# Performance work log

Measured on AMD Instinct MI355X. Metric: run time of the kernel, lower is better.

The kernel has to match this reference:

```python
import jax, jax.numpy as jnp
import numpy as np

B, L, Q, K, H = 64, 1024, 1024, 1024, 1024

def setup_inputs() -> dict:
    key = jax.random.key(0)
    k1, k2, k3, k4, k5, k6 = jax.random.split(key, 6)
    query = jax.random.normal(k1, (B, Q), dtype=jnp.float32)
    keys = jax.random.normal(k2, (B, L, K), dtype=jnp.float32)
    mask = jax.random.randint(k3, (B, L), 0, 2).astype(bool)
    # nn.Linear weights: W1 [H, Q], W2 [H, K], v [1, H], all bias-free
    W1 = jax.random.normal(k4, (H, Q), dtype=jnp.float32) / np.sqrt(Q)
    W2 = jax.random.normal(k5, (H, K), dtype=jnp.float32) / np.sqrt(K)
    v = jax.random.normal(k6, (1, H), dtype=jnp.float32) / np.sqrt(H)
    return {"query": query, "keys": keys, "mask": mask, "W1": W1, "W2": W2, "v": v}

def reference(query, keys, mask, W1, W2, v):
    # q: [B, H], broadcast over seq dim instead of expand
    q = query @ W1.T                                  # [B, H]
    k = jnp.einsum('blk,hk->blh', keys, W2)           # [B, L, H]
    scores = jnp.tanh(q[:, None, :] + k) @ v[0]       # [B, L]
    scores = jnp.where(mask, -jnp.inf, scores)
    weights = jax.nn.softmax(scores, axis=-1)
    weights = jnp.nan_to_num(weights, nan=0.0)
    context = jnp.einsum('bl,blk->bk', weights, keys) # [B, K]
    return (context, weights)
```

## Files before the change

### kernel.cpp

```cpp
#include <hip/hip_runtime.h>
#include <math.h>


typedef __attribute__((ext_vector_type(8))) short short8;
typedef __attribute__((ext_vector_type(4))) float floatx4;

__device__ __forceinline__ short f2bf(float x) {
    unsigned u = __float_as_uint(x);
    u += 0x7fffu + ((u >> 16) & 1u);
    return (short)(u >> 16);
}
__device__ __forceinline__ short8 pack8(float4 lo, float4 hi) {
    short8 r;
    r[0]=f2bf(lo.x); r[1]=f2bf(lo.y); r[2]=f2bf(lo.z); r[3]=f2bf(lo.w);
    r[4]=f2bf(hi.x); r[5]=f2bf(hi.y); r[6]=f2bf(hi.z); r[7]=f2bf(hi.w);
    return r;
}
__device__ __forceinline__ float fast_tanh(float x) {
    const float e = __expf(2.f * x);
    return 1.f - 2.f * __builtin_amdgcn_rcpf(e + 1.f);
}

#define LDA 40

__global__ __launch_bounds__(256) void k0_zero(float* __restrict__ out) {
    const int i = (blockIdx.x * 256 + threadIdx.x) * 4;
    const float4 z = {0.f, 0.f, 0.f, 0.f};
    *(float4*)(out + i) = z;
}

__global__ __launch_bounds__(256) void k1_qproj(
    const float* __restrict__ query, const float* __restrict__ W1,
    float* __restrict__ out)
{
    __shared__ float As[32][64];
    __shared__ float Bs[32][64];
    const int t  = threadIdx.x;
    const int tx = t & 15, ty = t >> 4;
    const int h0 = blockIdx.x * 64;
    const int kbase = blockIdx.y * 256;
    const int sr = t >> 2;
    const int sk = (t & 3) * 8;
    float c[4][4] = {{0.f}};
    for (int k0 = kbase; k0 < kbase + 256; k0 += 32) {
        const float4 a0 = *(const float4*)(query + sr * 1024 + k0 + sk);
        const float4 a1 = *(const float4*)(query + sr * 1024 + k0 + sk + 4);
        const float4 b0 = *(const float4*)(W1 + (h0 + sr) * 1024 + k0 + sk);
        const float4 b1 = *(const float4*)(W1 + (h0 + sr) * 1024 + k0 + sk + 4);
        __syncthreads();
        As[sk+0][sr]=a0.x; As[sk+1][sr]=a0.y; As[sk+2][sr]=a0.z; As[sk+3][sr]=a0.w;
        As[sk+4][sr]=a1.x; As[sk+5][sr]=a1.y; As[sk+6][sr]=a1.z; As[sk+7][sr]=a1.w;
        Bs[sk+0][sr]=b0.x; Bs[sk+1][sr]=b0.y; Bs[sk+2][sr]=b0.z; Bs[sk+3][sr]=b0.w;
        Bs[sk+4][sr]=b1.x; Bs[sk+5][sr]=b1.y; Bs[sk+6][sr]=b1.z; Bs[sk+7][sr]=b1.w;
        __syncthreads();
        #pragma unroll
        for (int k = 0; k < 32; ++k) {
            const float4 av = *(const float4*)&As[k][ty*4];
            const float4 bv = *(const float4*)&Bs[k][tx*4];
            const float aa[4] = {av.x, av.y, av.z, av.w};
            const float bb[4] = {bv.x, bv.y, bv.z, bv.w};
            #pragma unroll
            for (int i = 0; i < 4; ++i)
                #pragma unroll
                for (int j = 0; j < 4; ++j)
                    c[i][j] = fmaf(aa[i], bb[j], c[i][j]);
        }
    }
    #pragma unroll
    for (int i = 0; i < 4; ++i)
        #pragma unroll
        for (int j = 0; j < 4; ++j)
            atomicAdd(&out[(ty*4 + i) * 1024 + h0 + tx*4 + j], c[i][j]);
}

__global__ __launch_bounds__(256) void k_pack(const float* __restrict__ src,
                                              short* __restrict__ dst, int npanels)
{
    __shared__ short sm[16][1032];
    const int t = threadIdx.x;
    for (int p = blockIdx.x; p < npanels; p += gridDim.x) {
        const float* s = src + (size_t)p * 16 * 1024;
        short* d = dst + (size_t)p * 16 * 1024;
        __syncthreads();
        #pragma unroll
        for (int it = 0; it < 8; ++it) {
            const int idx = it * 256 + t;
            const int row = idx >> 7;
            const int c8  = idx & 127;
            const float4 a = *(const float4*)(s + row * 1024 + c8 * 8);
            const float4 b = *(const float4*)(s + row * 1024 + c8 * 8 + 4);
            *(short8*)&sm[row][c8 * 8] = pack8(a, b);
        }
        __syncthreads();
        #pragma unroll
        for (int it = 0; it < 8; ++it) {
            const int u = it * 256 + t;
            const int m = u & 15, c = u >> 4;
            ((short8*)d)[u] = *(const short8*)&sm[m][c * 8];
        }
    }
}

__global__ __launch_bounds__(256) void k2_scores_full(
    const short* __restrict__ keysp, const short* __restrict__ W2p,
    const float* __restrict__ v, float* __restrict__ out)
{
    __shared__ float red[128][33];
    const int t  = threadIdx.x;
    const int l0 = blockIdx.x * 128;
    const int b  = blockIdx.y;
    const int hz = blockIdx.z;
    const float* q = out;
    float* score = out + 65536;

    const int lane = t & 63, wid = t >> 6;
    const int quad = lane >> 4, m16 = lane & 15;
    const int wm = (wid >> 1) * 64;
    const int wn = (wid & 1) * 64;

    const short8* pA = (const short8*)keysp
        + ((size_t)(b * 64 + (l0 >> 4) + (wm >> 4))) * 2048 + quad * 16 + m16;

    float s_loc[4][4] = {{0.f}};

    for (int hb = hz * 4; hb < hz * 4 + 4; ++hb) {
        const short8* pB = (const short8*)W2p
            + ((size_t)(hb * 8 + (wn >> 4))) * 2048 + quad * 16 + m16;

        floatx4 acc[4][4] = {};
        short8 a0[4], b0[4], a1[4], b1[4];
        #pragma unroll
        for (int i = 0; i < 4; ++i) { a0[i] = pA[i * 2048]; b0[i] = pB[i * 2048]; }

        for (int kk = 0; kk < 928; kk += 64) {
            #pragma unroll
            for (int i = 0; i < 4; ++i) {
                a1[i] = pA[i * 2048 + (kk + 32) * 2];
                b1[i] = pB[i * 2048 + (kk + 32) * 2];
            }
            #pragma unroll
            for (int i = 0; i < 4; ++i)
                #pragma unroll
                for (int j = 0; j < 4; ++j)
                    acc[i][j] = __builtin_amdgcn_mfma_f32_16x16x32_bf16(a0[i], b0[j], acc[i][j], 0, 0, 0);
            #pragma unroll
            for (int i = 0; i < 4; ++i) {
                a0[i] = pA[i * 2048 + (kk + 64) * 2];
                b0[i] = pB[i * 2048 + (kk + 64) * 2];
            }
            #pragma unroll
            for (int i = 0; i < 4; ++i)
                #pragma unroll
                for (int j = 0; j < 4; ++j)
                    acc[i][j] = __builtin_amdgcn_mfma_f32_16x16x32_bf16(a1[i], b1[j], acc[i][j], 0, 0, 0);
        }
        #pragma unroll
        for (int i = 0; i < 4; ++i) {
            a1[i] = pA[i * 2048 + 992 * 2];
            b1[i] = pB[i * 2048 + 992 * 2];
        }
        #pragma unroll
        for (int i = 0; i < 4; ++i)
            #pragma unroll
            for (int j = 0; j < 4; ++j)
                acc[i][j] = __builtin_amdgcn_mfma_f32_16x16x32_bf16(a0[i], b0[j], acc[i][j], 0, 0, 0);
        #pragma unroll
        for (int i = 0; i < 4; ++i)
            #pragma unroll
            for (int j = 0; j < 4; ++j)
                acc[i][j] = __builtin_amdgcn_mfma_f32_16x16x32_bf16(a1[i], b1[j], acc[i][j], 0, 0, 0);

        float qv[4], vv[4];
        #pragma unroll
        for (int j = 0; j < 4; ++j) {
            const int h = hb * 128 + wn + j * 16 + m16;
            qv[j] = q[b * 1024 + h];
            vv[j] = v[h];
        }
        #pragma unroll
        for (int i = 0; i < 4; ++i)
            #pragma unroll
            for (int r = 0; r < 4; ++r) {
                float s = 0.f;
                #pragma unroll
                for (int j = 0; j < 4; ++j)
                    s += fast_tanh(qv[j] + acc[i][j][r]) * vv[j];
                s_loc[i][r] += s;
            }
    }

    #pragma unroll
    for (int i = 0; i < 4; ++i)
        #pragma unroll
        for (int r = 0; r < 4; ++r)
            red[wm + i * 16 + quad * 4 + r][(wid & 1) * 16 + m16] = s_loc[i][r];
    __syncthreads();
    if (t < 128) {
        const float* rr = red[t];
        float s = 0.f;
        #pragma unroll
        for (int c = 0; c < 32; ++c) s += rr[c];
        atomicAdd(&score[b * 1024 + l0 + t], s);
    }
}

__global__ __launch_bounds__(256) void k2_scores(
    const float* __restrict__ keys, const float* __restrict__ W2,
    const float* __restrict__ v, float* __restrict__ out)
{
    __shared__ union {
        struct { short A[128][LDA]; short B[128][LDA]; } st;
        float red[128][33];
    } sm;
    const int t  = threadIdx.x;
    const int hb = blockIdx.x;
    const int l0 = blockIdx.y * 128;
    const int b  = blockIdx.z;
    const int h0 = hb * 128;
    const float* q = out;
    float* score = out + 65536;

    const int srow = t >> 1;
    const int skh  = (t & 1) * 16;
    const float* Arow = keys + ((size_t)(b * 1024 + l0 + srow)) * 1024 + skh;
    const float* Brow = W2   + ((size_t)(h0 + srow)) * 1024 + skh;

    const int lane = t & 63, wid = t >> 6;
    const int quad = lane >> 4, m16 = lane & 15;
    const int wm = (wid >> 1) * 64;
    const int wn = (wid & 1) * 64;

    floatx4 acc[4][4] = {};

    for (int kk = 0; kk < 1024; kk += 32) {
        const float4 a0 = *(const float4*)(Arow + kk);
        const float4 a1 = *(const float4*)(Arow + kk + 4);
        const float4 a2 = *(const float4*)(Arow + kk + 8);
        const float4 a3 = *(const float4*)(Arow + kk + 12);
        const float4 w0 = *(const float4*)(Brow + kk);
        const float4 w1 = *(const float4*)(Brow + kk + 4);
        const float4 w2 = *(const float4*)(Brow + kk + 8);
        const float4 w3 = *(const float4*)(Brow + kk + 12);
        __syncthreads();
        *(short8*)&sm.st.A[srow][skh]     = pack8(a0, a1);
        *(short8*)&sm.st.A[srow][skh + 8] = pack8(a2, a3);
        *(short8*)&sm.st.B[srow][skh]     = pack8(w0, w1);
        *(short8*)&sm.st.B[srow][skh + 8] = pack8(w2, w3);
        __syncthreads();
        short8 af[4], bf[4];
        #pragma unroll
        for (int i = 0; i < 4; ++i)
            af[i] = *(const short8*)&sm.st.A[wm + i*16 + m16][quad * 8];
        #pragma unroll
        for (int j = 0; j < 4; ++j)
            bf[j] = *(const short8*)&sm.st.B[wn + j*16 + m16][quad * 8];
        #pragma unroll
        for (int i = 0; i < 4; ++i)
            #pragma unroll
            for (int j = 0; j < 4; ++j)
                acc[i][j] = __builtin_amdgcn_mfma_f32_16x16x32_bf16(af[i], bf[j], acc[i][j], 0, 0, 0);
    }

    float qv[4], vv[4];
    #pragma unroll
    for (int j = 0; j < 4; ++j) {
        const int h = h0 + wn + j * 16 + m16;
        qv[j] = q[b * 1024 + h];
        vv[j] = v[h];
    }
    __syncthreads();
    #pragma unroll
    for (int i = 0; i < 4; ++i) {
        #pragma unroll
        for (int r = 0; r < 4; ++r) {
            float s = 0.f;
            #pragma unroll
            for (int j = 0; j < 4; ++j)
                s += fast_tanh(qv[j] + acc[i][j][r]) * vv[j];
            sm.red[wm + i * 16 + quad * 4 + r][(wid & 1) * 16 + m16] = s;
        }
    }
    __syncthreads();
    if (t < 128) {
        const float* rr = sm.red[t];
        float s = 0.f;
        #pragma unroll
        for (int c = 0; c < 32; ++c) s += rr[c];
        atomicAdd(&score[b * 1024 + l0 + t], s);
    }
}

__global__ __launch_bounds__(256) void k3_softmax(
    const unsigned char* __restrict__ mask_u8, float* __restrict__ out)
{
    __shared__ float sc[1024];
    __shared__ float red[256];
    __shared__ int nz_sh;
    const int b = blockIdx.x;
    const int t = threadIdx.x;

    if (t == 0) nz_sh = 0;
    __syncthreads();
    {
        int nz = 0;
        #pragma unroll
        for (int j = 1; j < 4; ++j)
            if (mask_u8[t * 4 + j] != 0) nz = 1;
        if (nz) atomicAdd(&nz_sh, 1);
    }
    __syncthreads();
    const int use_i32 = (nz_sh == 0);
    const int* mask_i32 = (const int*)mask_u8;

    float* score = out + 65536;
    float lmax = -INFINITY;
    #pragma unroll
    for (int i = 0; i < 4; ++i) {
        const int l = t + i * 256;
        float s = score[b * 1024 + l];
        const int ml = b * 1024 + l;
        const bool masked = use_i32 ? (mask_i32[ml] != 0) : (mask_u8[ml] != 0);
        if (masked) s = -INFINITY;
        sc[l] = s;
        lmax = fmaxf(lmax, s);
    }
    red[t] = lmax;
    __syncthreads();
    for (int off = 128; off > 0; off >>= 1) {
        if (t < off) red[t] = fmaxf(red[t], red[t + off]);
        __syncthreads();
    }
    const float m = red[0];
    __syncthreads();
    float e[4];
    float lsum = 0.f;
    #pragma unroll
    for (int i = 0; i < 4; ++i) {
        const float s = sc[t + i * 256];
        const float ev = (s > -INFINITY && m > -INFINITY) ? expf(s - m) : 0.f;
        e[i] = ev;
        lsum += ev;
    }
    red[t] = lsum;
    __syncthreads();
    for (int off = 128; off > 0; off >>= 1) {
        if (t < off) red[t] += red[t + off];
        __syncthreads();
    }
    const float S = red[0];
    const float inv = (S > 0.f) ? (1.f / S) : 0.f;
    #pragma unroll
    for (int i = 0; i < 4; ++i)
        score[b * 1024 + t + i * 256] = e[i] * inv;
    const float4 z = {0.f, 0.f, 0.f, 0.f};
    ((float4*)(out + b * 1024))[t] = z;
}

__global__ __launch_bounds__(256) void k4_context(
    const float* __restrict__ keys, float* __restrict__ out)
{
    __shared__ float w[64];
    const int t  = threadIdx.x;
    const int b  = blockIdx.y;
    const int l0 = blockIdx.x * 64;
    if (t < 64) w[t] = out[65536 + b * 1024 + l0 + t];
    __syncthreads();
    const float4* kp = (const float4*)(keys + ((size_t)b * 1024 + (size_t)l0) * 1024) + t;
    float4 acc = {0.f, 0.f, 0.f, 0.f};
    #pragma unroll 4
    for (int l = 0; l < 64; ++l) {
        const float4 kv = kp[(size_t)l * 256];
        const float wv = w[l];
        acc.x = fmaf(wv, kv.x, acc.x);
        acc.y = fmaf(wv, kv.y, acc.y);
        acc.z = fmaf(wv, kv.z, acc.z);
        acc.w = fmaf(wv, kv.w, acc.w);
    }
    float* o = out + b * 1024 + t * 4;
    atomicAdd(o + 0, acc.x);
    atomicAdd(o + 1, acc.y);
    atomicAdd(o + 2, acc.z);
    atomicAdd(o + 3, acc.w);
}

extern "C" void kernel_launch(void* const* d_in, const int* in_sizes, int n_in,
                              void* d_out, int out_size, void* d_ws, size_t ws_size,
                              hipStream_t stream) {
    const float*         query = (const float*)d_in[0];
    const float*         keys  = (const float*)d_in[1];
    const unsigned char* mask  = (const unsigned char*)d_in[2];
    const float*         W1    = (const float*)d_in[3];
    const float*         W2    = (const float*)d_in[4];
    const float*         v     = (const float*)d_in[5];
    float* out = (float*)d_out;

    const size_t KEYS_BF = (size_t)64 * 1024 * 1024 * 2;
    const size_t W2_BF   = (size_t)1024 * 1024 * 2;
    const bool use_ws = (d_ws != nullptr) && (ws_size >= KEYS_BF + W2_BF);

    k0_zero   <<<dim3(128),       256, 0, stream>>>(out);
    k1_qproj  <<<dim3(16, 4),     256, 0, stream>>>(query, W1, out);
    if (use_ws) {
        short* keysp = (short*)d_ws;
        short* W2p   = keysp + KEYS_BF / 2;
        k_pack<<<dim3(4096), 256, 0, stream>>>(keys, keysp, 4096);
        k_pack<<<dim3(64),   256, 0, stream>>>(W2,   W2p,   64);
        k2_scores_full<<<dim3(8, 64, 2), 256, 0, stream>>>(keysp, W2p, v, out);
    } else {
        k2_scores<<<dim3(8, 8, 64), 256, 0, stream>>>(keys, W2, v, out);
    }
    k3_softmax<<<dim3(64),        256, 0, stream>>>(mask, out);
    k4_context<<<dim3(16, 64),    256, 0, stream>>>(keys, out);
}
```

Baseline: 669.0 us.

## Split scores GEMM over more H-blocks and reorder grid for key reuse

Result: slower. 705.3 us (+5.4%).

```diff
diff --git a/kernel.cpp b/kernel.cpp
--- a/kernel.cpp
+++ b/kernel.cpp
@@ -101,15 +101,15 @@
     }
 }
 
-__global__ __launch_bounds__(256) void k2_scores_full(
+__global__ __launch_bounds__(256, 3) void k2_scores_full(
     const short* __restrict__ keysp, const short* __restrict__ W2p,
     const float* __restrict__ v, float* __restrict__ out)
 {
     __shared__ float red[128][33];
     const int t  = threadIdx.x;
-    const int l0 = blockIdx.x * 128;
-    const int b  = blockIdx.y;
-    const int hz = blockIdx.z;
+    const int hz = blockIdx.x;
+    const int l0 = blockIdx.y * 128;
+    const int b  = blockIdx.z;
     const float* q = out;
     float* score = out + 65536;
 
@@ -118,25 +118,35 @@
     const int wm = (wid >> 1) * 64;
     const int wn = (wid & 1) * 64;
 
-    const short8* pA = (const short8*)keysp
-        + ((size_t)(b * 64 + (l0 >> 4) + (wm >> 4))) * 2048 + quad * 16 + m16;
+    const int loff = (quad * 16 + m16) * 8;
+    const int apan = __builtin_amdgcn_readfirstlane(b * 64 + (l0 >> 4) + (wm >> 4));
 
     float s_loc[4][4] = {{0.f}};
 
-    for (int hb = hz * 4; hb < hz * 4 + 4; ++hb) {
-        const short8* pB = (const short8*)W2p
-            + ((size_t)(hb * 8 + (wn >> 4))) * 2048 + quad * 16 + m16;
+    for (int p = 0; p < 2; ++p) {
+        const int hb = hz * 2 + p;
+        const int bpan = __builtin_amdgcn_readfirstlane(hb * 8 + (wn >> 4));
+        const short* ab[4];
+        const short* bb[4];
+        #pragma unroll
+        for (int i = 0; i < 4; ++i) {
+            ab[i] = keysp + (size_t)(apan + i) * 16384;
+            bb[i] = W2p  + (size_t)(bpan + i) * 16384;
+        }
 
         floatx4 acc[4][4] = {};
         short8 a0[4], b0[4], a1[4], b1[4];
         #pragma unroll
-        for (int i = 0; i < 4; ++i) { a0[i] = pA[i * 2048]; b0[i] = pB[i * 2048]; }
-
-        for (int kk = 0; kk < 928; kk += 64) {
+        for (int i = 0; i < 4; ++i) {
+            a0[i] = *(const short8*)(ab[i] + loff);
+            b0[i] = *(const short8*)(bb[i] + loff);
+        }
+
+        for (int w = 0; w < 15; ++w) {
             #pragma unroll
             for (int i = 0; i < 4; ++i) {
-                a1[i] = pA[i * 2048 + (kk + 32) * 2];
-                b1[i] = pB[i * 2048 + (kk + 32) * 2];
+                a1[i] = *(const short8*)(ab[i] + loff + 512);
+                b1[i] = *(const short8*)(bb[i] + loff + 512);
             }
             #pragma unroll
             for (int i = 0; i < 4; ++i)
@@ -145,19 +155,21 @@
                     acc[i][j] = __builtin_amdgcn_mfma_f32_16x16x32_bf16(a0[i], b0[j], acc[i][j], 0, 0, 0);
             #pragma unroll
             for (int i = 0; i < 4; ++i) {
-                a0[i] = pA[i * 2048 + (kk + 64) * 2];
-                b0[i] = pB[i * 2048 + (kk + 64) * 2];
+                a0[i] = *(const short8*)(ab[i] + loff + 1024);
+                b0[i] = *(const short8*)(bb[i] + loff + 1024);
             }
             #pragma unroll
             for (int i = 0; i < 4; ++i)
                 #pragma unroll
                 for (int j = 0; j < 4; ++j)
                     acc[i][j] = __builtin_amdgcn_mfma_f32_16x16x32_bf16(a1[i], b1[j], acc[i][j], 0, 0, 0);
+            #pragma unroll
+            for (int i = 0; i < 4; ++i) { ab[i] += 1024; bb[i] += 1024; }
         }
         #pragma unroll
         for (int i = 0; i < 4; ++i) {
-            a1[i] = pA[i * 2048 + 992 * 2];
-            b1[i] = pB[i * 2048 + 992 * 2];
+            a1[i] = *(const short8*)(ab[i] + loff + 512);
+            b1[i] = *(const short8*)(bb[i] + loff + 512);
         }
         #pragma unroll
         for (int i = 0; i < 4; ++i)
@@ -405,7 +417,7 @@
         short* W2p   = keysp + KEYS_BF / 2;
         k_pack<<<dim3(4096), 256, 0, stream>>>(keys, keysp, 4096);
         k_pack<<<dim3(64),   256, 0, stream>>>(W2,   W2p,   64);
-        k2_scores_full<<<dim3(8, 64, 2), 256, 0, stream>>>(keysp, W2p, v, out);
+        k2_scores_full<<<dim3(4, 8, 64), 256, 0, stream>>>(keysp, W2p, v, out);
     } else {
         k2_scores<<<dim3(8, 8, 64), 256, 0, stream>>>(keys, W2, v, out);
     }
```

## Stage full keys tile in LDS via direct global-to-LDS loads in score kernel

Applied to the files above, without the earlier changes.

New measurement: 1.101 ms. +64.5%, slower.

```diff
diff --git a/kernel.cpp b/kernel.cpp
--- a/kernel.cpp
+++ b/kernel.cpp
@@ -20,6 +20,11 @@
     const float e = __expf(2.f * x);
     return 1.f - 2.f * __builtin_amdgcn_rcpf(e + 1.f);
 }
+__device__ __forceinline__ void gload_lds16(const short* g, short* l) {
+    __builtin_amdgcn_global_load_lds(
+        (const __attribute__((address_space(1))) unsigned int*)g,
+        (__attribute__((address_space(3))) unsigned int*)l, 16, 0, 0);
+}
 
 #define LDA 40
 
@@ -27,6 +32,11 @@
     const int i = (blockIdx.x * 256 + threadIdx.x) * 4;
     const float4 z = {0.f, 0.f, 0.f, 0.f};
     *(float4*)(out + i) = z;
+}
+__global__ __launch_bounds__(256) void k0_zero_score(float* __restrict__ out) {
+    const int i = (blockIdx.x * 256 + threadIdx.x) * 4;
+    const float4 z = {0.f, 0.f, 0.f, 0.f};
+    *(float4*)(out + 65536 + i) = z;
 }
 
 __global__ __launch_bounds__(256) void k1_qproj(
@@ -38,11 +48,11 @@
     const int t  = threadIdx.x;
     const int tx = t & 15, ty = t >> 4;
     const int h0 = blockIdx.x * 64;
-    const int kbase = blockIdx.y * 256;
+    const int kbase = blockIdx.y * 128;
     const int sr = t >> 2;
     const int sk = (t & 3) * 8;
     float c[4][4] = {{0.f}};
-    for (int k0 = kbase; k0 < kbase + 256; k0 += 32) {
+    for (int k0 = kbase; k0 < kbase + 128; k0 += 32) {
         const float4 a0 = *(const float4*)(query + sr * 1024 + k0 + sk);
         const float4 a1 = *(const float4*)(query + sr * 1024 + k0 + sk + 4);
         const float4 b0 = *(const float4*)(W1 + (h0 + sr) * 1024 + k0 + sk);
@@ -101,106 +111,90 @@
     }
 }
 
-__global__ __launch_bounds__(256) void k2_scores_full(
+__global__ __launch_bounds__(1024) void k2_scores_lds(
     const short* __restrict__ keysp, const short* __restrict__ W2p,
     const float* __restrict__ v, float* __restrict__ out)
 {
-    __shared__ float red[128][33];
+    __shared__ union {
+        short A[65536];
+        float red[64][65];
+    } sm;
     const int t  = threadIdx.x;
-    const int l0 = blockIdx.x * 128;
+    const int l0 = blockIdx.x * 64;
     const int b  = blockIdx.y;
-    const int hz = blockIdx.z;
     const float* q = out;
     float* score = out + 65536;
 
     const int lane = t & 63, wid = t >> 6;
     const int quad = lane >> 4, m16 = lane & 15;
-    const int wm = (wid >> 1) * 64;
-    const int wn = (wid & 1) * 64;
-
-    const short8* pA = (const short8*)keysp
-        + ((size_t)(b * 64 + (l0 >> 4) + (wm >> 4))) * 2048 + quad * 16 + m16;
-
-    float s_loc[4][4] = {{0.f}};
-
-    for (int hb = hz * 4; hb < hz * 4 + 4; ++hb) {
-        const short8* pB = (const short8*)W2p
-            + ((size_t)(hb * 8 + (wn >> 4))) * 2048 + quad * 16 + m16;
-
-        floatx4 acc[4][4] = {};
-        short8 a0[4], b0[4], a1[4], b1[4];
-        #pragma unroll
-        for (int i = 0; i < 4; ++i) { a0[i] = pA[i * 2048]; b0[i] = pB[i * 2048]; }
-
-        for (int kk = 0; kk < 928; kk += 64) {
-            #pragma unroll
-            for (int i = 0; i < 4; ++i) {
-                a1[i] = pA[i * 2048 + (kk + 32) * 2];
-                b1[i] = pB[i * 2048 + (kk + 32) * 2];
-            }
-            #pragma unroll
-            for (int i = 0; i < 4; ++i)
-                #pragma unroll
-                for (int j = 0; j < 4; ++j)
-                    acc[i][j] = __builtin_amdgcn_mfma_f32_16x16x32_bf16(a0[i], b0[j], acc[i][j], 0, 0, 0);
-            #pragma unroll
-            for (int i = 0; i < 4; ++i) {
-                a0[i] = pA[i * 2048 + (kk + 64) * 2];
-                b0[i] = pB[i * 2048 + (kk + 64) * 2];
-            }
-            #pragma unroll
-            for (int i = 0; i < 4; ++i)
-                #pragma unroll
-                for (int j = 0; j < 4; ++j)
-                    acc[i][j] = __builtin_amdgcn_mfma_f32_16x16x32_bf16(a1[i], b1[j], acc[i][j], 0, 0, 0);
+    const int wM = wid >> 2;
+    const int wN = wid & 3;
+
+    const size_t abase = (size_t)(b * 64 + (l0 >> 4)) * 16384;
+    #pragma unroll
+    for (int it = 0; it < 8; ++it) {
+        const int u = it * 1024 + t;
+        gload_lds16(keysp + abase + (size_t)u * 8, sm.A + u * 8);
+    }
+    __syncthreads();
+
+    const int aoff = wM * 16384 + quad * 128 + m16 * 8;
+    const int boff = quad * 128 + m16 * 8;
+
+    float s_loc[4] = {0.f, 0.f, 0.f, 0.f};
+
+    for (int hb = 0; hb < 8; ++hb) {
+        const short* Bp0 = W2p + (size_t)(hb * 8 + wN * 2)     * 16384 + boff;
+        const short* Bp1 = W2p + (size_t)(hb * 8 + wN * 2 + 1) * 16384 + boff;
+
+        floatx4 acc0 = {}, acc1 = {};
+        short8 a0, a1, b00, b10, b01, b11;
+        a0  = *(const short8*)&sm.A[aoff];
+        b00 = *(const short8*)Bp0;
+        b10 = *(const short8*)Bp1;
+
+        for (int w = 0; w < 15; ++w) {
+            const int wk = w * 1024;
+            a1  = *(const short8*)&sm.A[aoff + wk + 512];
+            b01 = *(const short8*)(Bp0 + 512);
+            b11 = *(const short8*)(Bp1 + 512);
+            acc0 = __builtin_amdgcn_mfma_f32_16x16x32_bf16(a0, b00, acc0, 0, 0, 0);
+            acc1 = __builtin_amdgcn_mfma_f32_16x16x32_bf16(a0, b10, acc1, 0, 0, 0);
+            a0  = *(const short8*)&sm.A[aoff + wk + 1024];
+            b00 = *(const short8*)(Bp0 + 1024);
+            b10 = *(const short8*)(Bp1 + 1024);
+            acc0 = __builtin_amdgcn_mfma_f32_16x16x32_bf16(a1, b01, acc0, 0, 0, 0);
+            acc1 = __builtin_amdgcn_mfma_f32_16x16x32_bf16(a1, b11, acc1, 0, 0, 0);
+            Bp0 += 1024; Bp1 += 1024;
         }
-        #pragma unroll
-        for (int i = 0; i < 4; ++i) {
-            a1[i] = pA[i * 2048 + 992 * 2];
-            b1[i] = pB[i * 2048 + 992 * 2];
-        }
-        #pragma unroll
-        for (int i = 0; i < 4; ++i)
-            #pragma unroll
-            for (int j = 0; j < 4; ++j)
-                acc[i][j] = __builtin_amdgcn_mfma_f32_16x16x32_bf16(a0[i], b0[j], acc[i][j], 0, 0, 0);
-        #pragma unroll
-        for (int i = 0; i < 4; ++i)
-            #pragma unroll
-            for (int j = 0; j < 4; ++j)
-                acc[i][j] = __builtin_amdgcn_mfma_f32_16x16x32_bf16(a1[i], b1[j], acc[i][j], 0, 0, 0);
-
-        float qv[4], vv[4];
-        #pragma unroll
-        for (int j = 0; j < 4; ++j) {
-            const int h = hb * 128 + wn + j * 16 + m16;
-            qv[j] = q[b * 1024 + h];
-            vv[j] = v[h];
-        }
-        #pragma unroll
-        for (int i = 0; i < 4; ++i)
-            #pragma unroll
-            for (int r = 0; r < 4; ++r) {
-                float s = 0.f;
-                #pragma unroll
-                for (int j = 0; j < 4; ++j)
-                    s += fast_tanh(qv[j] + acc[i][j][r]) * vv[j];
-                s_loc[i][r] += s;
-            }
-    }
-
-    #pragma unroll
-    for (int i = 0; i < 4; ++i)
+        a1  = *(const short8*)&sm.A[aoff + 15 * 1024 + 512];
+        b01 = *(const short8*)(Bp0 + 512);
+        b11 = *(const short8*)(Bp1 + 512);
+        acc0 = __builtin_amdgcn_mfma_f32_16x16x32_bf16(a0, b00, acc0, 0, 0, 0);
+        acc1 = __builtin_amdgcn_mfma_f32_16x16x32_bf16(a0, b10, acc1, 0, 0, 0);
+        acc0 = __builtin_amdgcn_mfma_f32_16x16x32_bf16(a1, b01, acc0, 0, 0, 0);
+        acc1 = __builtin_amdgcn_mfma_f32_16x16x32_bf16(a1, b11, acc1, 0, 0, 0);
+
+        const int h = hb * 128 + wN * 32 + m16;
+        const float qv0 = q[b * 1024 + h],      vv0 = v[h];
+        const float qv1 = q[b * 1024 + h + 16], vv1 = v[h + 16];
         #pragma unroll
         for (int r = 0; r < 4; ++r)
-            red[wm + i * 16 + quad * 4 + r][(wid & 1) * 16 + m16] = s_loc[i][r];
-    __syncthreads();
-    if (t < 128) {
-        const float* rr = red[t];
+            s_loc[r] += fast_tanh(qv0 + acc0[r]) * vv0
+                      + fast_tanh(qv1 + acc1[r]) * vv1;
+    }
+
+    __syncthreads();
+    #pragma unroll
+    for (int r = 0; r < 4; ++r)
+        sm.red[wM * 16 + quad * 4 + r][wN * 16 + m16] = s_loc[r];
+    __syncthreads();
+    if (t < 64) {
+        const float* rr = sm.red[t];
         float s = 0.f;
         #pragma unroll
-        for (int c = 0; c < 32; ++c) s += rr[c];
-        atomicAdd(&score[b * 1024 + l0 + t], s);
+        for (int c = 0; c < 64; ++c) s += rr[c];
+        score[b * 1024 + l0 + t] = s;
     }
 }
 
@@ -398,15 +392,16 @@
     const size_t W2_BF   = (size_t)1024 * 1024 * 2;
     const bool use_ws = (d_ws != nullptr) && (ws_size >= KEYS_BF + W2_BF);
 
-    k0_zero   <<<dim3(128),       256, 0, stream>>>(out);
-    k1_qproj  <<<dim3(16, 4),     256, 0, stream>>>(query, W1, out);
+    k0_zero   <<<dim3(64),        256, 0, stream>>>(out);
+    k1_qproj  <<<dim3(16, 8),     256, 0, stream>>>(query, W1, out);
     if (use_ws) {
         short* keysp = (short*)d_ws;
         short* W2p   = keysp + KEYS_BF / 2;
         k_pack<<<dim3(4096), 256, 0, stream>>>(keys, keysp, 4096);
         k_pack<<<dim3(64),   256, 0, stream>>>(W2,   W2p,   64);
-        k2_scores_full<<<dim3(8, 64, 2), 256, 0, stream>>>(keysp, W2p, v, out);
+        k2_scores_lds<<<dim3(16, 64), 1024, 0, stream>>>(keysp, W2p, v, out);
     } else {
+        k0_zero_score<<<dim3(64), 256, 0, stream>>>(out);
         k2_scores<<<dim3(8, 8, 64), 256, 0, stream>>>(keys, W2, v, out);
     }
     k3_softmax<<<dim3(64),        256, 0, stream>>>(mask, out);
```
